# Kernel tuning notes

Hardware: AMD Instinct MI355X
Metric: run time of the kernel (lower is better)

Reference implementation:

```python
import jax, jax.numpy as jnp
import numpy as np

C = 64
CR = C // 8  # reduced channels for Q/K


def _conv1x1(x, W, b):
    # 1x1 conv == per-pixel linear over channels: x [b,c,h,w], W [o,c], b [o]
    return jnp.einsum('bchw,oc->bohw', x, W) + b[None, :, None, None]


def setup_inputs() -> dict:
    key = jax.random.key(0)
    ks = jax.random.split(key, 12)
    b, c, h, w = 8, C, 48, 48
    s = 1.0 / np.sqrt(c)
    inp = {
        'x1': jax.random.normal(ks[0], (b, c, h, w), jnp.float32),
        'x2': jax.random.normal(ks[1], (b, c, h, w), jnp.float32),
        'Wqk1': jax.random.normal(ks[2], (2 * CR, c), jnp.float32) * s,
        'bqk1': jnp.zeros((2 * CR,), jnp.float32),
        'Wqk2': jax.random.normal(ks[3], (2 * CR, c), jnp.float32) * s,
        'bqk2': jnp.zeros((2 * CR,), jnp.float32),
        'Wv1': jax.random.normal(ks[4], (c, c), jnp.float32) * s,
        'bv1': jnp.zeros((c,), jnp.float32),
        'Wv2': jax.random.normal(ks[5], (c, c), jnp.float32) * s,
        'bv2': jnp.zeros((c,), jnp.float32),
        'gamma': jnp.zeros((1,), jnp.float32) + 0.1,  # nonzero so output depends on attn
        'beta': jnp.zeros((1,), jnp.float32) + 0.1,
    }
    return inp


def reference(x1, x2, Wqk1, bqk1, Wqk2, bqk2, Wv1, bv1, Wv2, bv2, gamma, beta):
    b, c, h, w = x1.shape
    n = h * w
    qk1 = _conv1x1(x1, Wqk1, bqk1)
    qk2 = _conv1x1(x2, Wqk2, bqk2)
    q1, k1 = qk1[:, :CR], qk1[:, CR:]
    q2, k2 = qk2[:, :CR], qk2[:, CR:]
    # flatten spatial: [b, cr, n]
    q1 = q1.reshape(b, CR, n); k1 = k1.reshape(b, CR, n)
    q2 = q2.reshape(b, CR, n); k2 = k2.reshape(b, CR, n)
    v1 = _conv1x1(x1, Wv1, bv1).reshape(b, c, n)
    v2 = _conv1x1(x2, Wv2, bv2).reshape(b, c, n)
    # attn[b,i,j] = softmax_j( q[:, :, i] . k[:, :, j] )
    attn1 = jax.nn.softmax(jnp.einsum('bci,bcj->bij', q1, k1), axis=-1)
    attn2 = jax.nn.softmax(jnp.einsum('bci,bcj->bij', q2, k2), axis=-1)
    # out[:, :, j] = sum_i v[:, :, i] * attn[:, i, j]
    o1 = jnp.einsum('bci,bij->bcj', v1, attn2).reshape(b, c, h, w) * gamma + x1
    o2 = jnp.einsum('bci,bij->bcj', v2, attn1).reshape(b, c, h, w) * beta + x2
    return (o1, o2)
```

## Files before the change

kernel.cpp:

```cpp
#include <hip/hip_runtime.h>
#include <hip/hip_bf16.h>

#define NB   8
#define CCH  64
#define CR8  8
#define NPX  2304
#define BCN  (NB*CCH*NPX)
#define LOG2E 1.4426950408889634f

typedef short  short8   __attribute__((ext_vector_type(8)));
typedef unsigned short ushort8t __attribute__((ext_vector_type(8)));
typedef float  float4t  __attribute__((ext_vector_type(4)));
typedef float  float16t __attribute__((ext_vector_type(16)));

static __device__ __forceinline__ float fexp2(float x) {
    return __builtin_amdgcn_exp2f(x);
}
static __device__ __forceinline__ unsigned short bf16r(float f) {
    return (unsigned short)((__float_as_uint(f) + 0x8000u) >> 16);
}
static __device__ __forceinline__ unsigned int pack_bf16(float lo, float hi) {
    const unsigned int ul = __float_as_uint(lo) + 0x8000u;
    const unsigned int uh = __float_as_uint(hi) + 0x8000u;
    return __builtin_amdgcn_perm(uh, ul, 0x07060302u);
}
static __device__ __forceinline__ short8 pack8(const float* f) {
    union { unsigned int u[4]; short8 s; } r;
    #pragma unroll
    for (int j = 0; j < 4; j++) r.u[j] = pack_bf16(f[2*j], f[2*j+1]);
    return r.s;
}

static __device__ __forceinline__ void build_bfrag(const float16t sc, short8* bf) {
    unsigned int d[4][2];
    #pragma unroll
    for (int q = 0; q < 4; q++) {
        #pragma unroll
        for (int m = 0; m < 2; m++)
            d[q][m] = pack_bf16(fexp2(sc[4*q + 2*m]), fexp2(sc[4*q + 2*m + 1]));
    }
    #pragma unroll
    for (int kp = 0; kp < 2; kp++) {
        union { unsigned int u[4]; short8 s; } r;
        #pragma unroll
        for (int m = 0; m < 2; m++) {
            unsigned int x = d[2*kp][m];
            unsigned int y = d[2*kp + 1][m];
            asm("v_permlane32_swap_b32 %0, %1" : "+v"(x), "+v"(y));
            r.u[m]     = x;
            r.u[2 + m] = y;
        }
        bf[kp] = r.s;
    }
}

#define WS_QB1 0
#define WS_KB1 (WS_QB1 + 147456)
#define WS_QB2 (WS_KB1 + 147456)
#define WS_KB2 (WS_QB2 + 147456)
#define WS_V1  (WS_KB2 + 147456)
#define WS_V2  (WS_V1 + BCN/2)

__global__ __launch_bounds__(256) void proj_kernel(
    const float* __restrict__ x1, const float* __restrict__ x2,
    const float* __restrict__ Wqk1, const float* __restrict__ bqk1,
    const float* __restrict__ Wqk2, const float* __restrict__ bqk2,
    const float* __restrict__ Wv1,  const float* __restrict__ bv1,
    const float* __restrict__ Wv2,  const float* __restrict__ bv2,
    float* __restrict__ ws, float* __restrict__ out)
{
    const int t    = threadIdx.x;
    const int lane = t & 63;
    const int w    = t >> 6;
    const int n16  = lane & 15;
    const int c4   = lane >> 4;
    const int nt   = w & 1;
    const int mh   = w >> 1;
    const int b    = blockIdx.y;
    const int px   = blockIdx.x * 32 + nt * 16 + n16;

    const float* xsb[2];
    xsb[0] = x1 + ((size_t)b * CCH) * NPX + px;
    xsb[1] = x2 + ((size_t)b * CCH) * NPX + px;

    float xr[2][16];
    short8 bfrag[2][2];
    #pragma unroll
    for (int st = 0; st < 2; st++) {
        #pragma unroll
        for (int ch = 0; ch < 2; ch++) {
            #pragma unroll
            for (int j = 0; j < 8; j++)
                xr[st][ch * 8 + j] = xsb[st][(ch * 32 + c4 * 8 + j) * NPX];
            bfrag[st][ch] = pack8(&xr[st][ch * 8]);
        }
    }

    if (mh == 0) {
        #pragma unroll
        for (int st = 0; st < 2; st++) {
            float* outs = out + (st ? (size_t)BCN : 0);
            #pragma unroll
            for (int e = 0; e < 16; e++) {
                const int ch = (e >> 3) * 32 + c4 * 8 + (e & 7);
                outs[((size_t)b * CCH + ch) * NPX + px] = xr[st][e];
            }
        }
    }

    float4t acc[5];
    #pragma unroll
    for (int mt = 0; mt < 5; mt++) { acc[mt][0]=0.f; acc[mt][1]=0.f; acc[mt][2]=0.f; acc[mt][3]=0.f; }

    #pragma unroll
    for (int mt = 0; mt < 5; mt++) {
        const int mi  = mh * 5 + mt;
        const int isqk = (mi < 2);
        const int st  = isqk ? (mi & 1) : (mi >= 6);
        const float* Wb;
        int rowbase;
        if (isqk) { Wb = (mi == 0) ? Wqk1 : Wqk2; rowbase = 0; }
        else      { Wb = (mi >= 6) ? Wv2 : Wv1; rowbase = (mi - (mi >= 6 ? 6 : 2)) * 16; }
        const float* wrow = Wb + (size_t)(rowbase + n16) * 64 + c4 * 8;

        const short8 bf0 = st ? bfrag[1][0] : bfrag[0][0];
        const short8 bf1 = st ? bfrag[1][1] : bfrag[0][1];

        #pragma unroll
        for (int ch = 0; ch < 2; ch++) {
            float fa[8];
            const float4 a0 = *(const float4*)(wrow + ch * 32);
            const float4 a1 = *(const float4*)(wrow + ch * 32 + 4);
            fa[0] = a0.x; fa[1] = a0.y; fa[2] = a0.z; fa[3] = a0.w;
            fa[4] = a1.x; fa[5] = a1.y; fa[6] = a1.z; fa[7] = a1.w;
            acc[mt] = __builtin_amdgcn_mfma_f32_16x16x32_bf16(
                pack8(fa), ch ? bf1 : bf0, acc[mt], 0, 0, 0);
        }
    }

    #pragma unroll
    for (int mt = 0; mt < 5; mt++) {
        const int mi = mh * 5 + mt;
        if (mi < 2) {
            const int st = mi & 1;
            const float* bqk = st ? bqk2 : bqk1;
            unsigned short* qb = (unsigned short*)(ws + (st ? WS_QB2 : WS_QB1));
            unsigned short* kb = (unsigned short*)(ws + (st ? WS_KB2 : WS_KB1));
            const size_t rbase = (size_t)(b * NPX + px) * 16;
            #pragma unroll
            for (int r = 0; r < 4; r++) {
                const int oc = c4 * 4 + r;
                const float val = acc[mt][r] + bqk[oc];
                if (oc < 8)
                    qb[rbase + oc] = bf16r(val * LOG2E);
                else
                    kb[rbase + (oc - 8)] = bf16r(val);
            }
            ushort8t zq, zk;
            #pragma unroll
            for (int e = 0; e < 8; e++) { zq[e] = 0; zk[e] = 0; }
            zk[0] = 0x3F80; zk[1] = 0x3F80;
            if (c4 == 0) *(ushort8t*)(qb + rbase + 8) = zq;
            if (c4 == 2) *(ushort8t*)(kb + rbase + 8) = zk;
        } else {
            const int st = (mi >= 6);
            const int vt_ = mi - (st ? 6 : 2);
            const float* bv = st ? bv2 : bv1;
            unsigned short* v = (unsigned short*)(ws + (st ? WS_V2 : WS_V1));
            #pragma unroll
            for (int r = 0; r < 4; r++) {
                const int oc = vt_ * 16 + c4 * 4 + r;
                const float val = acc[mt][r] + bv[oc];
                v[((size_t)b * CCH + oc) * NPX + px] = bf16r(val);
            }
        }
    }
}

__global__ __launch_bounds__(256) void stats_kernel(float* __restrict__ ws)
{
    const int t  = threadIdx.x;
    const int w  = t >> 6;
    const int n  = t & 31;
    const int h  = (t & 63) >> 5;
    const int ig = blockIdx.x;
    const int ab = blockIdx.y;
    const int b  = ab & 7;
    const int a  = ab >> 3;

    unsigned short* qbw = (unsigned short*)(ws + (a ? WS_QB2 : WS_QB1));
    const unsigned short* qb = qbw;
    const unsigned short* kb = (const unsigned short*)(ws + (a ? WS_KB2 : WS_KB1));

    __shared__ float red[4][32];

    const short8 qf = *(const short8*)(qb + (size_t)(b * NPX + ig * 32 + n) * 16 + h * 8);

    const unsigned short* kp = kb + (size_t)(b * NPX + w * 576 + n) * 16 + h * 8;
    short8 kf = *(const short8*)kp;

    float ssum = 0.f;
    for (int jc = 0; jc < 18; jc++) {
        kp += 512;
        short8 kn = kf;
        if (jc + 1 < 18) kn = *(const short8*)kp;
        float16t acc = {};
        __builtin_amdgcn_s_setprio(1);
        acc = __builtin_amdgcn_mfma_f32_32x32x16_bf16(kf, qf, acc, 0, 0, 0);
        __builtin_amdgcn_s_setprio(0);
        float s0 = 0.f, s1 = 0.f, s2 = 0.f, s3 = 0.f;
        #pragma unroll
        for (int r = 0; r < 4; r++) {
            s0 += fexp2(acc[4 * r + 0]);
            s1 += fexp2(acc[4 * r + 1]);
            s2 += fexp2(acc[4 * r + 2]);
            s3 += fexp2(acc[4 * r + 3]);
        }
        ssum += (s0 + s1) + (s2 + s3);
        kf = kn;
    }
    ssum += __shfl_xor(ssum, 32);
    if (h == 0) red[w][n] = ssum;
    __syncthreads();

    if (t < 32) {
        const float d = (red[0][t] + red[1][t]) + (red[2][t] + red[3][t]);
        const float m = -__log2f(d);
        const unsigned short mhi = bf16r(m);
        __hip_bfloat16 hb; *(unsigned short*)&hb = mhi;
        const unsigned short mlo = bf16r(m - __bfloat162float(hb));
        const size_t rbase = (size_t)(b * NPX + ig * 32 + t) * 16;
        qbw[rbase + 8] = mhi;
        qbw[rbase + 9] = mlo;
    }
}

__global__ __launch_bounds__(256) void out_kernel(
    const float* __restrict__ gamma, const float* __restrict__ beta,
    const float* __restrict__ ws, float* __restrict__ out)
{
    const int t  = threadIdx.x;
    const int jt = blockIdx.x;
    const int b  = blockIdx.y;
    const int z  = blockIdx.z;
    const int o  = z >> 1;
    const int g  = z & 1;

    const int a = o ? 0 : 1;
    const unsigned short* qb = (const unsigned short*)(ws + (a ? WS_QB2 : WS_QB1));
    const unsigned short* kb = (const unsigned short*)(ws + (a ? WS_KB2 : WS_KB1));
    const unsigned short* v  = (const unsigned short*)(ws + (o ? WS_V2 : WS_V1));
    const float  scale = o ? beta[0] : gamma[0];

    __shared__ unsigned short vt[2][64][72];

    const int lane = t & 63;
    const int w    = t >> 6;
    const int n    = lane & 31;
    const int h    = lane >> 5;
    const int jh   = w & 1;
    const int ih   = w >> 1;

    const int j0 = jt * 64 + jh * 32;

    const short8 kfrag = *(const short8*)(kb + (size_t)(b * NPX + j0 + n) * 16 + h * 8);

    const int c0 = t >> 3, s80 = (t & 7) * 8;
    const int c1 = (t + 256) >> 3, s81 = ((t + 256) & 7) * 8;

    const int ibase = g * 1152;
    const unsigned short* vp0 = v + ((size_t)b * CCH + c0) * NPX + ibase + s80;
    const unsigned short* vp1 = v + ((size_t)b * CCH + c1) * NPX + ibase + s81;
    const unsigned short* qp  = qb + (size_t)(b * NPX + ibase + ih * 32 + n) * 16 + h * 8;

    {
        const float4 va = *(const float4*)vp0;
        const float4 vb = *(const float4*)vp1;
        *(float4*)&vt[0][c0][s80] = va;
        *(float4*)&vt[0][c1][s81] = vb;
    }
    short8 qf = *(const short8*)qp;

    float16t oacc0 = {}, oacc1 = {};
    int cur = 0;

    for (int it = 0; it < 18; it++) {
        vp0 += 64; vp1 += 64; qp += 64 * 16;
        float4 vn0, vn1;
        short8 qn = qf;
        if (it + 1 < 18) {
            vn0 = *(const float4*)vp0;
            vn1 = *(const float4*)vp1;
            qn  = *(const short8*)qp;
        }

        __syncthreads();

        float16t sc = {};
        __builtin_amdgcn_s_setprio(1);
        sc = __builtin_amdgcn_mfma_f32_32x32x16_bf16(qf, kfrag, sc, 0, 0, 0);
        __builtin_amdgcn_s_setprio(0);

        short8 bf[2];
        build_bfrag(sc, bf);

        {
            const short8 a0 = *(const short8*)&vt[cur][n][ih * 32 + 0 * 16 + h * 8];
            const short8 a1 = *(const short8*)&vt[cur][32 + n][ih * 32 + 0 * 16 + h * 8];
            __builtin_amdgcn_s_setprio(1);
            oacc0 = __builtin_amdgcn_mfma_f32_32x32x16_bf16(a0, bf[0], oacc0, 0, 0, 0);
            oacc1 = __builtin_amdgcn_mfma_f32_32x32x16_bf16(a1, bf[0], oacc1, 0, 0, 0);
            __builtin_amdgcn_s_setprio(0);
            const short8 a2 = *(const short8*)&vt[cur][n][ih * 32 + 1 * 16 + h * 8];
            const short8 a3 = *(const short8*)&vt[cur][32 + n][ih * 32 + 1 * 16 + h * 8];
            __builtin_amdgcn_s_setprio(1);
            oacc0 = __builtin_amdgcn_mfma_f32_32x32x16_bf16(a2, bf[1], oacc0, 0, 0, 0);
            oacc1 = __builtin_amdgcn_mfma_f32_32x32x16_bf16(a3, bf[1], oacc1, 0, 0, 0);
            __builtin_amdgcn_s_setprio(0);
        }

        if (it + 1 < 18) {
            *(float4*)&vt[cur ^ 1][c0][s80] = vn0;
            *(float4*)&vt[cur ^ 1][c1][s81] = vn1;
        }

        qf = qn;
        cur ^= 1;
    }

    __syncthreads();
    float* comb = (float*)&vt[0][0][0];
    float* cb = comb + (size_t)jh * 2304 + (size_t)lane * 36;
    if (ih == 1) {
        *(float4*)(cb +  0) = *((const float4*)&oacc0 + 0);
        *(float4*)(cb +  4) = *((const float4*)&oacc0 + 1);
        *(float4*)(cb +  8) = *((const float4*)&oacc0 + 2);
        *(float4*)(cb + 12) = *((const float4*)&oacc0 + 3);
        *(float4*)(cb + 16) = *((const float4*)&oacc1 + 0);
        *(float4*)(cb + 20) = *((const float4*)&oacc1 + 1);
        *(float4*)(cb + 24) = *((const float4*)&oacc1 + 2);
        *(float4*)(cb + 28) = *((const float4*)&oacc1 + 3);
    }
    __syncthreads();
    if (ih == 0) {
        #pragma unroll
        for (int q = 0; q < 4; q++) {
            const float4 p0 = *(const float4*)(cb + q * 4);
            const float4 p1 = *(const float4*)(cb + 16 + q * 4);
            oacc0[4*q+0] += p0.x; oacc0[4*q+1] += p0.y; oacc0[4*q+2] += p0.z; oacc0[4*q+3] += p0.w;
            oacc1[4*q+0] += p1.x; oacc1[4*q+1] += p1.y; oacc1[4*q+2] += p1.z; oacc1[4*q+3] += p1.w;
        }
        float* outp = out + (o ? BCN : 0) + (b * CCH) * NPX + j0 + n;
        #pragma unroll
        for (int r = 0; r < 16; r++) {
            const int row = (r & 3) + 8 * (r >> 2) + 4 * h;
            atomicAdd(outp + row * NPX, oacc0[r] * scale);
            atomicAdd(outp + (32 + row) * NPX, oacc1[r] * scale);
        }
    }
}

extern "C" void kernel_launch(void* const* d_in, const int* in_sizes, int n_in,
                              void* d_out, int out_size, void* d_ws, size_t ws_size,
                              hipStream_t stream)
{
    const float* x1   = (const float*)d_in[0];
    const float* x2   = (const float*)d_in[1];
    const float* Wqk1 = (const float*)d_in[2];
    const float* bqk1 = (const float*)d_in[3];
    const float* Wqk2 = (const float*)d_in[4];
    const float* bqk2 = (const float*)d_in[5];
    const float* Wv1  = (const float*)d_in[6];
    const float* bv1  = (const float*)d_in[7];
    const float* Wv2  = (const float*)d_in[8];
    const float* bv2  = (const float*)d_in[9];
    const float* gamma = (const float*)d_in[10];
    const float* beta  = (const float*)d_in[11];
    float* out = (float*)d_out;
    float* ws  = (float*)d_ws;

    proj_kernel<<<dim3(72, 8), 256, 0, stream>>>(
        x1, x2, Wqk1, bqk1, Wqk2, bqk2, Wv1, bv1, Wv2, bv2, ws, out);
    stats_kernel<<<dim3(72, 16), 256, 0, stream>>>(ws);
    out_kernel<<<dim3(36, 8, 4), 256, 0, stream>>>(gamma, beta, ws, out);
}
```

Baseline: 135.8 us.

## Give each wave a private V tile in LDS to drop per-iteration block barriers

The 64-pixel V tile that all four waves shared through double-buffered LDS is replaced by a separate 64x32 slice per wave, loaded directly into that wave's own LDS region. Since each wave now only reads data it wrote itself, the __syncthreads inside the 18-step loop goes away and waves no longer stall waiting for each other. In exchange, the two waves covering the same pixel half each load the same V data, so global/L2 reads of V double. Each wave also issues four 16-byte loads per step instead of two.

```diff
diff --git a/kernel.cpp b/kernel.cpp
--- a/kernel.cpp
+++ b/kernel.cpp
@@ -252,7 +252,7 @@
     const unsigned short* v  = (const unsigned short*)(ws + (o ? WS_V2 : WS_V1));
     const float  scale = o ? beta[0] : gamma[0];
 
-    __shared__ unsigned short vt[2][64][72];
+    __shared__ unsigned short vt[4][64][36];
 
     const int lane = t & 63;
     const int w    = t >> 6;
@@ -265,36 +265,47 @@
 
     const short8 kfrag = *(const short8*)(kb + (size_t)(b * NPX + j0 + n) * 16 + h * 8);
 
-    const int c0 = t >> 3, s80 = (t & 7) * 8;
-    const int c1 = (t + 256) >> 3, s81 = ((t + 256) & 7) * 8;
-
-    const int ibase = g * 1152;
-    const unsigned short* vp0 = v + ((size_t)b * CCH + c0) * NPX + ibase + s80;
-    const unsigned short* vp1 = v + ((size_t)b * CCH + c1) * NPX + ibase + s81;
-    const unsigned short* qp  = qb + (size_t)(b * NPX + ibase + ih * 32 + n) * 16 + h * 8;
-
-    {
-        const float4 va = *(const float4*)vp0;
-        const float4 vb = *(const float4*)vp1;
-        *(float4*)&vt[0][c0][s80] = va;
-        *(float4*)&vt[0][c1][s81] = vb;
-    }
+    const int ibase = g * 1152 + ih * 32;
+
+    const int id0 = lane,        c_0 = id0 >> 2, o_0 = (id0 & 3) * 8;
+    const int id1 = 64  + lane,  c_1 = id1 >> 2, o_1 = (id1 & 3) * 8;
+    const int id2 = 128 + lane,  c_2 = id2 >> 2, o_2 = (id2 & 3) * 8;
+    const int id3 = 192 + lane,  c_3 = id3 >> 2, o_3 = (id3 & 3) * 8;
+    const unsigned short* s0p = v + ((size_t)b * CCH + c_0) * NPX + ibase + o_0;
+    const unsigned short* s1p = v + ((size_t)b * CCH + c_1) * NPX + ibase + o_1;
+    const unsigned short* s2p = v + ((size_t)b * CCH + c_2) * NPX + ibase + o_2;
+    const unsigned short* s3p = v + ((size_t)b * CCH + c_3) * NPX + ibase + o_3;
+    unsigned short* d0 = &vt[w][c_0][o_0];
+    unsigned short* d1 = &vt[w][c_1][o_1];
+    unsigned short* d2 = &vt[w][c_2][o_2];
+    unsigned short* d3 = &vt[w][c_3][o_3];
+
+    const unsigned short* qp = qb + (size_t)(b * NPX + ibase + n) * 16 + h * 8;
+
+    float4 vc0 = *(const float4*)s0p;
+    float4 vc1 = *(const float4*)s1p;
+    float4 vc2 = *(const float4*)s2p;
+    float4 vc3 = *(const float4*)s3p;
     short8 qf = *(const short8*)qp;
 
     float16t oacc0 = {}, oacc1 = {};
-    int cur = 0;
 
     for (int it = 0; it < 18; it++) {
-        vp0 += 64; vp1 += 64; qp += 64 * 16;
-        float4 vn0, vn1;
+        s0p += 64; s1p += 64; s2p += 64; s3p += 64; qp += 64 * 16;
+        float4 vn0, vn1, vn2, vn3;
         short8 qn = qf;
         if (it + 1 < 18) {
-            vn0 = *(const float4*)vp0;
-            vn1 = *(const float4*)vp1;
+            vn0 = *(const float4*)s0p;
+            vn1 = *(const float4*)s1p;
+            vn2 = *(const float4*)s2p;
+            vn3 = *(const float4*)s3p;
             qn  = *(const short8*)qp;
         }
 
-        __syncthreads();
+        *(float4*)d0 = vc0;
+        *(float4*)d1 = vc1;
+        *(float4*)d2 = vc2;
+        *(float4*)d3 = vc3;
 
         float16t sc = {};
         __builtin_amdgcn_s_setprio(1);
@@ -305,27 +316,22 @@
         build_bfrag(sc, bf);
 
         {
-            const short8 a0 = *(const short8*)&vt[cur][n][ih * 32 + 0 * 16 + h * 8];
-            const short8 a1 = *(const short8*)&vt[cur][32 + n][ih * 32 + 0 * 16 + h * 8];
+            const short8 a0 = *(const short8*)&vt[w][n][h * 8];
+            const short8 a1 = *(const short8*)&vt[w][32 + n][h * 8];
             __builtin_amdgcn_s_setprio(1);
             oacc0 = __builtin_amdgcn_mfma_f32_32x32x16_bf16(a0, bf[0], oacc0, 0, 0, 0);
             oacc1 = __builtin_amdgcn_mfma_f32_32x32x16_bf16(a1, bf[0], oacc1, 0, 0, 0);
             __builtin_amdgcn_s_setprio(0);
-            const short8 a2 = *(const short8*)&vt[cur][n][ih * 32 + 1 * 16 + h * 8];
-            const short8 a3 = *(const short8*)&vt[cur][32 + n][ih * 32 + 1 * 16 + h * 8];
+            const short8 a2 = *(const short8*)&vt[w][n][16 + h * 8];
+            const short8 a3 = *(const short8*)&vt[w][32 + n][16 + h * 8];
             __builtin_amdgcn_s_setprio(1);
             oacc0 = __builtin_amdgcn_mfma_f32_32x32x16_bf16(a2, bf[1], oacc0, 0, 0, 0);
             oacc1 = __builtin_amdgcn_mfma_f32_32x32x16_bf16(a3, bf[1], oacc1, 0, 0, 0);
             __builtin_amdgcn_s_setprio(0);
         }
 
-        if (it + 1 < 18) {
-            *(float4*)&vt[cur ^ 1][c0][s80] = vn0;
-            *(float4*)&vt[cur ^ 1][c1][s81] = vn1;
-        }
-
+        vc0 = vn0; vc1 = vn1; vc2 = vn2; vc3 = vn3;
         qf = qn;
-        cur ^= 1;
     }
 
     __syncthreads();
```

After: 156.7 us. +15.4%, slower.
